# Optimization experiments

Hardware: AMD Instinct MI355X
Metric: run time of the kernel (lower is better)

The kernel has to match this reference:

```python
import jax, jax.numpy as jnp
import numpy as np

NA, NW, H = 20000, 100000, 128
DA, DW = 64, 128
E_CR, E_IN, E_CO = 400000, 600000, 300000


def _seg_softmax(logits, seg, n):
    m = jax.ops.segment_max(logits, seg, num_segments=n)
    e = jnp.exp(logits - m[seg])
    s = jax.ops.segment_sum(e, seg, num_segments=n)
    return e / (s[seg] + 1e-16)


def _gat(x_src, x_dst, edge, W, b, a_s, a_d):
    # PyG GATConv, heads=1, concat=False, shared lin for src/dst, add_self_loops=True
    n_src, n_dst = x_src.shape[0], x_dst.shape[0]
    loops = jnp.arange(min(n_src, n_dst), dtype=edge.dtype)
    src = jnp.concatenate([edge[0], loops])
    dst = jnp.concatenate([edge[1], loops])
    hs = x_src @ W            # [n_src, H]
    hd = x_dst @ W            # [n_dst, H]
    logit = jax.nn.leaky_relu((hs @ a_s)[src] + (hd @ a_d)[dst], 0.2)
    alpha = _seg_softmax(logit, dst, n_dst)          # softmax over in-neighborhoods
    out = jax.ops.segment_sum(alpha[:, None] * hs[src], dst, num_segments=n_dst)
    return out + b


def _mlp2(x, w1, b1, w2, b2):
    return jax.nn.relu(x @ w1 + b1) @ w2 + b2


def setup_inputs() -> dict:
    key = jax.random.key(0)
    ks = iter(jax.random.split(key, 40))

    def p(shape, scale=0.1):
        return jax.random.normal(next(ks), shape, jnp.float32) * scale

    def edges(n_src, n_dst, E):
        s = jax.random.randint(next(ks), (E,), 0, n_src, dtype=jnp.int32)
        d = jax.random.randint(next(ks), (E,), 0, n_dst, dtype=jnp.int32)
        d = jnp.where(s == d, (d + 1) % n_dst, d)  # keep input loop-free (PyG strips them)
        return jnp.stack([s, d])

    e_creates = edges(NA, NW, E_CR)
    inp = {
        'artist_feat': jax.random.normal(next(ks), (NA, DA), jnp.float32),
        'work_feat': jax.random.normal(next(ks), (NW, DW), jnp.float32),
        'a_w1': p((DA, H)), 'a_b1': jnp.zeros(H, jnp.float32),
        'a_w2': p((H, H)), 'a_b2': jnp.zeros(H, jnp.float32),
        'w_w1': p((DW, H)), 'w_b1': jnp.zeros(H, jnp.float32),
        'w_w2': p((H, H)), 'w_b2': jnp.zeros(H, jnp.float32),
        'cr_W': p((H, H)), 'cr_b': jnp.zeros(H, jnp.float32), 'cr_as': p((H,)), 'cr_ad': p((H,)),
        'in_W': p((H, H)), 'in_b': jnp.zeros(H, jnp.float32), 'in_as': p((H,)), 'in_ad': p((H,)),
        'co_W': p((H, H)), 'co_b': jnp.zeros(H, jnp.float32), 'co_as': p((H,)), 'co_ad': p((H,)),
        'p_w1': p((2 * H, 256)), 'p_b1': jnp.zeros(256, jnp.float32),
        'p_w2': p((256, 128)), 'p_b2': jnp.zeros(128, jnp.float32),
        'p_w3': p((128, 1)), 'p_b3': jnp.zeros(1, jnp.float32),
        'e_creates': e_creates,
        'e_created_by': jnp.flip(e_creates, axis=0),  # reverse relation [work, artist]
        'e_infl': edges(NW, NW, E_IN),
        'e_collab': edges(NA, NA, E_CO),
    }
    return inp


def reference(artist_feat, work_feat,
              a_w1, a_b1, a_w2, a_b2,
              w_w1, w_b1, w_w2, w_b2,
              cr_W, cr_b, cr_as, cr_ad,
              in_W, in_b, in_as, in_ad,
              co_W, co_b, co_as, co_ad,
              p_w1, p_b1, p_w2, p_b2, p_w3, p_b3,
              e_creates, e_created_by, e_infl, e_collab):
    ax = _mlp2(artist_feat, a_w1, a_b1, a_w2, a_b2)      # [NA, H]
    wx = _mlp2(work_feat, w_w1, w_b1, w_w2, w_b2)        # [NW, H]
    wx = jax.nn.elu(_gat(ax, wx, e_creates, cr_W, cr_b, cr_as, cr_ad))
    wx = jax.nn.elu(_gat(wx, wx, e_infl, in_W, in_b, in_as, in_ad))
    au = _gat(wx, ax, e_created_by, cr_W, cr_b, cr_as, cr_ad)  # no elu (matches source)
    ac = jax.nn.elu(_gat(au, au, e_collab, co_W, co_b, co_as, co_ad))
    comb = jnp.concatenate([au, ac], axis=1)             # [NA, 2H]
    h = jax.nn.relu(comb @ p_w1 + p_b1)                  # dropout is identity in eval
    h = jax.nn.relu(h @ p_w2 + p_b2)
    return (h @ p_w3 + p_b3).squeeze()
```

## Files before the change

kernel.cpp:

```cpp
#include <hip/hip_runtime.h>
#include <hip/hip_bf16.h>
#include <cstddef>

#define NA 20000
#define NW 100000
#define HH 128
#define DA 64
#define E_CR 400000
#define E_IN 600000
#define E_CO 300000

#define ROW1 0
#define ROW2 (NW)
#define ROW3 (2 * NW)
#define ROW4 (2 * NW + NA)
#define NTOT (2 * NW + 2 * NA)
#define CAPW 40
#define CAPA 88
#define NPREP (10 * 128 + 1)
#define GNB ((NA + 127) / 128)

typedef short v8s __attribute__((ext_vector_type(8)));
typedef float v4f __attribute__((ext_vector_type(4)));

constexpr int PSLOT = 2 * 128 * 264;

__device__ inline short f2bf(float x) {
    union { float f; unsigned u; } c; c.f = x;
    unsigned r = c.u + 0x7fff + ((c.u >> 16) & 1);
    return (short)(r >> 16);
}
__device__ inline float bf2f(short s) {
    union { unsigned u; float f; } c; c.u = ((unsigned)(unsigned short)s) << 16;
    return c.f;
}
__device__ inline float bfu2f(unsigned short s) {
    union { unsigned u; float f; } c; c.u = ((unsigned)s) << 16;
    return c.f;
}

__device__ inline void split8(const float* xv, v8s& h, v8s& l) {
#pragma unroll
    for (int p = 0; p < 4; ++p) {
        float2 xf; xf.x = xv[2 * p]; xf.y = xv[2 * p + 1];
        __hip_bfloat162 hb = __float22bfloat162_rn(xf);
        float2 hf = __bfloat1622float2(hb);
        float2 lf; lf.x = xf.x - hf.x; lf.y = xf.y - hf.y;
        __hip_bfloat162 lb = __float22bfloat162_rn(lf);
        union { __hip_bfloat162 b; short2 s; } uh, ul;
        uh.b = hb; ul.b = lb;
        h[2 * p] = uh.s.x; h[2 * p + 1] = uh.s.y;
        l[2 * p] = ul.s.x; l[2 * p + 1] = ul.s.y;
    }
}

struct AppChunk { const int* e; int E; int* pad; int cap; int* deg; };

__device__ inline void do_append(const AppChunk& ap, int bid) {
    int b0 = bid * 1024 + threadIdx.x;
    int s[4], d[4]; bool ok[4];
#pragma unroll
    for (int u = 0; u < 4; ++u) {
        int i = b0 + u * 256;
        ok[u] = i < ap.E;
        s[u] = 0; d[u] = 0;
        if (ok[u]) { s[u] = ap.e[i]; d[u] = ap.e[ap.E + i]; }
    }
    int p[4];
#pragma unroll
    for (int u = 0; u < 4; ++u) if (ok[u]) p[u] = atomicAdd(&ap.deg[d[u]], 1);
#pragma unroll
    for (int u = 0; u < 4; ++u)
        if (ok[u] && p[u] < ap.cap)
            ap.pad[(size_t)d[u] * ap.cap + p[u]] = s[u];
}

struct PrepDesc { const float* src; int ldw; int K; };
struct PrepArgs {
    PrepDesc d[10]; const float* wvW; const float* wvA; float* vd;
    const float* gX; const float* gB; float* gY; int gM;
};

__global__ __launch_bounds__(256) void k_prep_append(PrepArgs a, short* __restrict__ out,
                                                    AppChunk ap)
{
    __shared__ short Bs2[2 * 128 * 72];
    const int napp = (ap.E + 1023) >> 10;
    int bx = blockIdx.x;
    if (bx < napp) { do_append(ap, bx); return; }
    bx -= napp;
    if (bx < GNB) {
        const int bid = bx;
        const int tid = threadIdx.x;
        const int wave = tid >> 6, lane = tid & 63;
        const int l15 = lane & 15, quad = lane >> 4;
        const int wrow = bid * 128 + wave * 32;
        for (int e = tid; e < 64 * 128; e += 256) {
            int n = e & 127, k = e >> 7;
            float x = a.d[0].src[(size_t)k * 128 + n];
            short h = f2bf(x);
            short l = f2bf(x - bf2f(h));
            Bs2[n * 72 + k] = h;
            Bs2[128 * 72 + n * 72 + k] = l;
        }
        v8s ah[2][2], al[2][2];
#pragma unroll
        for (int rf = 0; rf < 2; ++rf) {
            int r = wrow + rf * 16 + l15; if (r >= a.gM) r = a.gM - 1;
            const float* xp = a.gX + (size_t)r * DA + quad * 8;
#pragma unroll
            for (int kf = 0; kf < 2; ++kf) {
                float xv[8];
                *(float4*)&xv[0] = *(const float4*)(xp + kf * 32);
                *(float4*)&xv[4] = *(const float4*)(xp + kf * 32 + 4);
                split8(xv, ah[rf][kf], al[rf][kf]);
            }
        }
        __syncthreads();
        v4f acc[2][8];
#pragma unroll
        for (int rf = 0; rf < 2; ++rf)
#pragma unroll
            for (int cf = 0; cf < 8; ++cf) acc[rf][cf] = (v4f){0.f, 0.f, 0.f, 0.f};
#pragma unroll
        for (int kf = 0; kf < 2; ++kf) {
#pragma unroll
            for (int cf = 0; cf < 8; ++cf) {
                int coff = (cf * 16 + l15) * 72 + kf * 32 + quad * 8;
                v8s bh = *(const v8s*)&Bs2[coff];
                v8s bl = *(const v8s*)&Bs2[128 * 72 + coff];
#pragma unroll
                for (int rf = 0; rf < 2; ++rf) {
                    acc[rf][cf] = __builtin_amdgcn_mfma_f32_16x16x32_bf16(al[rf][kf], bh, acc[rf][cf], 0, 0, 0);
                    acc[rf][cf] = __builtin_amdgcn_mfma_f32_16x16x32_bf16(ah[rf][kf], bl, acc[rf][cf], 0, 0, 0);
                    acc[rf][cf] = __builtin_amdgcn_mfma_f32_16x16x32_bf16(ah[rf][kf], bh, acc[rf][cf], 0, 0, 0);
                }
            }
        }
        float bv[8];
#pragma unroll
        for (int cf = 0; cf < 8; ++cf) bv[cf] = a.gB[cf * 16 + l15];
#pragma unroll
        for (int rf = 0; rf < 2; ++rf) {
#pragma unroll
            for (int reg = 0; reg < 4; ++reg) {
                int r = wrow + rf * 16 + quad * 4 + reg;
                if (r >= a.gM) continue;
                float* yp = a.gY + (size_t)r * HH;
#pragma unroll
                for (int cf = 0; cf < 8; ++cf) {
                    float o = acc[rf][cf][reg] + bv[cf];
                    yp[cf * 16 + l15] = o > 0.f ? o : 0.f;
                }
            }
        }
        return;
    }
    bx -= GNB;
    if (bx == NPREP - 1) {
        __shared__ float sa[HH];
        int t = threadIdx.x;
        if (t < HH) sa[t] = a.wvA[t];
        __syncthreads();
        if (t < HH) {
            float s = 0.f;
            for (int jj = 0; jj < HH; ++jj) s += a.wvW[(size_t)t * HH + jj] * sa[jj];
            a.vd[t] = s;
        }
        return;
    }
    int m = bx >> 7;
    int e = (bx & 127) * 256 + threadIdx.x;
    PrepDesc dd = a.d[m];
    int K = dd.K;
    int KP = (K <= 128) ? K + 8 : K;
    if (e >= K * 128) return;
    int n = e & 127, k = e >> 7;
    float x = dd.src[(size_t)k * dd.ldw + n];
    short h = f2bf(x);
    short l = f2bf(x - bf2f(h));
    short* base = out + (size_t)m * PSLOT;
    base[n * KP + k] = h;
    base[128 * KP + n * KP + k] = l;
}

template<int K, int ACT, int NSS, int ST, int LDSB, int OBF, int DUAL, int XBF>
__global__ __launch_bounds__(256, 4) void k_mfma(
    const float* __restrict__ X, int ldx,
    const short* __restrict__ Wp,
    const float* __restrict__ bias,
    float* __restrict__ Y, int ldy, int M,
    const float* __restrict__ v1, float* __restrict__ ss1,
    const float* __restrict__ v2, float* __restrict__ ss2,
    const float* __restrict__ sb)
{
    constexpr int KF = K / 32;
    constexpr int KP = (K <= 128) ? K + 8 : K;
    __shared__ short Bs[LDSB ? 2 * 128 * KP : 8];
    const int tid = threadIdx.x;
    const int wave = tid >> 6, lane = tid & 63;
    const int l15 = lane & 15, quad = lane >> 4;
    int bid = blockIdx.x;
    if (DUAL) {
        int g0 = gridDim.x >> 1;
        if (bid >= g0) { bid -= g0; Wp += PSLOT; bias += 128; Y += 128; }
    }
    const int wrow = bid * 128 + wave * 32;

    if (LDSB) {
        const float4* src = (const float4*)Wp;
        float4* dst = (float4*)Bs;
        constexpr int total = 2 * 128 * KP / 8;
        for (int i = tid; i < total; i += 256) dst[i] = src[i];
        __syncthreads();
    }

    v4f acc[2][8];
#pragma unroll
    for (int rf = 0; rf < 2; ++rf)
#pragma unroll
        for (int cf = 0; cf < 8; ++cf) acc[rf][cf] = (v4f){0.f, 0.f, 0.f, 0.f};

    const unsigned short* xb16[2];
    const float* xb32[2];
#pragma unroll
    for (int rf = 0; rf < 2; ++rf) {
        int r = wrow + rf * 16 + l15; if (r >= M) r = M - 1;
        xb16[rf] = (const unsigned short*)X + (size_t)r * ldx + quad * 8;
        xb32[rf] = X + (size_t)r * ldx + quad * 8;
    }

#pragma unroll
    for (int kf = 0; kf < KF; ++kf) {
        v8s ah[2], al[2];
#pragma unroll
        for (int rf = 0; rf < 2; ++rf) {
            if (XBF) {
                ah[rf] = *(const v8s*)(xb16[rf] + kf * 32);
            } else {
                float xv[8];
                *(float4*)&xv[0] = *(const float4*)(xb32[rf] + kf * 32);
                *(float4*)&xv[4] = *(const float4*)(xb32[rf] + kf * 32 + 4);
                split8(xv, ah[rf], al[rf]);
            }
        }
#pragma unroll
        for (int cf = 0; cf < 8; ++cf) {
            const short* bp = LDSB ? &Bs[(cf * 16 + l15) * KP + kf * 32 + quad * 8]
                                   : Wp + (size_t)(cf * 16 + l15) * KP + kf * 32 + quad * 8;
            v8s bh = *(const v8s*)bp;
            v8s bl = *(const v8s*)(bp + 128 * KP);
#pragma unroll
            for (int rf = 0; rf < 2; ++rf) {
                if (!XBF) acc[rf][cf] = __builtin_amdgcn_mfma_f32_16x16x32_bf16(al[rf], bh, acc[rf][cf], 0, 0, 0);
                acc[rf][cf] = __builtin_amdgcn_mfma_f32_16x16x32_bf16(ah[rf], bl, acc[rf][cf], 0, 0, 0);
                acc[rf][cf] = __builtin_amdgcn_mfma_f32_16x16x32_bf16(ah[rf], bh, acc[rf][cf], 0, 0, 0);
            }
        }
    }

    float bv[8], v1c[8], v2c[8];
#pragma unroll
    for (int cf = 0; cf < 8; ++cf) {
        int col = cf * 16 + l15;
        bv[cf] = bias ? bias[col] : 0.f;
        if (NSS >= 1) v1c[cf] = v1[col];
        if (NSS >= 2) v2c[cf] = v2[col];
    }
    float sbv = (NSS >= 1 && sb) ? sb[0] : 0.f;

#pragma unroll
    for (int rf = 0; rf < 2; ++rf) {
#pragma unroll
        for (int reg = 0; reg < 4; ++reg) {
            int r = wrow + rf * 16 + quad * 4 + reg;
            if (r >= M) continue;
            float p1 = 0.f, p2 = 0.f;
#pragma unroll
            for (int cf = 0; cf < 8; ++cf) {
                float o = acc[rf][cf][reg] + bv[cf];
                if (ACT == 1) o = o > 0.f ? o : 0.f;
                if (NSS >= 1) p1 = fmaf(o, v1c[cf], p1);
                if (NSS >= 2) p2 = fmaf(o, v2c[cf], p2);
                if (ST) {
                    if (OBF) ((unsigned short*)Y)[(size_t)r * ldy + cf * 16 + l15] = (unsigned short)f2bf(o);
                    else     Y[(size_t)r * ldy + cf * 16 + l15] = o;
                }
            }
            if (NSS >= 1) {
#pragma unroll
                for (int w = 1; w < 16; w <<= 1) {
                    p1 += __shfl_xor(p1, w, 64);
                    if (NSS >= 2) p2 += __shfl_xor(p2, w, 64);
                }
                if (l15 == 0) {
                    ss1[r] = p1 + sbv;
                    if (NSS >= 2) ss2[r] = p2;
                }
            }
        }
    }
}

struct MfmaCfg {
    const float* X; int ldx;
    const short* Wp;
    const float* bias;
    float* Y; int ldy; int M;
    int act, nss, obf, xbf, st;
    const float* v1; float* ss1;
    const float* v2; float* ss2;
    int nblocks;
};

__global__ __launch_bounds__(256, 4) void k_mfma2(MfmaCfg c0, MfmaCfg c1, AppChunk ap)
{
    constexpr int KF = 4, KP = 136;
    const int napp = (ap.E + 1023) >> 10;
    int bid = blockIdx.x;
    if (bid < napp) { do_append(ap, bid); return; }
    bid -= napp;
    const bool first = bid < c0.nblocks;
    const MfmaCfg& c = first ? c0 : c1;
    if (!first) bid -= c0.nblocks;
    const int tid = threadIdx.x;
    const int wave = tid >> 6, lane = tid & 63;
    const int l15 = lane & 15, quad = lane >> 4;
    const int wrow = bid * 128 + wave * 32;

    v4f acc[2][8];
#pragma unroll
    for (int rf = 0; rf < 2; ++rf)
#pragma unroll
        for (int cf = 0; cf < 8; ++cf) acc[rf][cf] = (v4f){0.f, 0.f, 0.f, 0.f};

    const unsigned short* xb16[2];
    const float* xb32[2];
#pragma unroll
    for (int rf = 0; rf < 2; ++rf) {
        int r = wrow + rf * 16 + l15; if (r >= c.M) r = c.M - 1;
        xb16[rf] = (const unsigned short*)c.X + (size_t)r * c.ldx + quad * 8;
        xb32[rf] = c.X + (size_t)r * c.ldx + quad * 8;
    }

#pragma unroll
    for (int kf = 0; kf < KF; ++kf) {
        v8s ah[2], al[2];
#pragma unroll
        for (int rf = 0; rf < 2; ++rf) {
            if (c.xbf) {
                ah[rf] = *(const v8s*)(xb16[rf] + kf * 32);
                al[rf] = (v8s)(short)0;
            } else {
                float xv[8];
                *(float4*)&xv[0] = *(const float4*)(xb32[rf] + kf * 32);
                *(float4*)&xv[4] = *(const float4*)(xb32[rf] + kf * 32 + 4);
                split8(xv, ah[rf], al[rf]);
            }
        }
#pragma unroll
        for (int cf = 0; cf < 8; ++cf) {
            const short* bp = c.Wp + (size_t)(cf * 16 + l15) * KP + kf * 32 + quad * 8;
            v8s bh = *(const v8s*)bp;
            v8s bl = *(const v8s*)(bp + 128 * KP);
#pragma unroll
            for (int rf = 0; rf < 2; ++rf) {
                if (!c.xbf) acc[rf][cf] = __builtin_amdgcn_mfma_f32_16x16x32_bf16(al[rf], bh, acc[rf][cf], 0, 0, 0);
                acc[rf][cf] = __builtin_amdgcn_mfma_f32_16x16x32_bf16(ah[rf], bl, acc[rf][cf], 0, 0, 0);
                acc[rf][cf] = __builtin_amdgcn_mfma_f32_16x16x32_bf16(ah[rf], bh, acc[rf][cf], 0, 0, 0);
            }
        }
    }

    float bv[8], v1c[8], v2c[8];
#pragma unroll
    for (int cf = 0; cf < 8; ++cf) {
        int col = cf * 16 + l15;
        bv[cf] = c.bias ? c.bias[col] : 0.f;
        v1c[cf] = (c.nss >= 1) ? c.v1[col] : 0.f;
        v2c[cf] = (c.nss >= 2) ? c.v2[col] : 0.f;
    }

#pragma unroll
    for (int rf = 0; rf < 2; ++rf) {
#pragma unroll
        for (int reg = 0; reg < 4; ++reg) {
            int r = wrow + rf * 16 + quad * 4 + reg;
            if (r >= c.M) continue;
            float p1 = 0.f, p2 = 0.f;
#pragma unroll
            for (int cf = 0; cf < 8; ++cf) {
                float o = acc[rf][cf][reg] + bv[cf];
                if (c.act) o = o > 0.f ? o : 0.f;
                p1 = fmaf(o, v1c[cf], p1);
                p2 = fmaf(o, v2c[cf], p2);
                if (c.st) {
                    if (c.obf) ((unsigned short*)c.Y)[(size_t)r * c.ldy + cf * 16 + l15] = (unsigned short)f2bf(o);
                    else       c.Y[(size_t)r * c.ldy + cf * 16 + l15] = o;
                }
            }
            if (c.nss >= 1) {
#pragma unroll
                for (int w = 1; w < 16; w <<= 1) {
                    p1 += __shfl_xor(p1, w, 64);
                    p2 += __shfl_xor(p2, w, 64);
                }
                if (l15 == 0) {
                    c.ss1[r] = p1;
                    if (c.nss >= 2) c.ss2[r] = p2;
                }
            }
        }
    }
}

template<int ELU, int U, int CAP, int OBF>
__global__ __launch_bounds__(256) void k_aggregate(
    const int* __restrict__ deg, const int* __restrict__ esp,
    const unsigned short* __restrict__ hs, const float* __restrict__ ss,
    const float* __restrict__ sd, const float* __restrict__ bias,
    void* __restrict__ out, int ldy, int n, int loopn)
{
    int lane = threadIdx.x & 63;
    int wv = threadIdx.x >> 6;
    int d = blockIdx.x * 4 + wv;
    if (d >= n) return;
    int half = lane >> 5;
    int col = (lane & 31) * 4;
    const int* row = esp + (size_t)d * CAP;
    int i1 = deg[d]; if (i1 > CAP) i1 = CAP;
    float sdv = sd[d];
    float den = 0.f;
    float ax = 0.f, ay = 0.f, az = 0.f, aw = 0.f;
    if (half == 0 && d < loopn) {
        ushort4 h = *(const ushort4*)(hs + (size_t)d * HH + col);
        float l = ss[d] + sdv;
        l = l < 0.f ? 0.2f * l : l;
        float e = __expf(l);
        den += e;
        ax = fmaf(e, bfu2f(h.x), ax);
        ay = fmaf(e, bfu2f(h.y), ay);
        az = fmaf(e, bfu2f(h.z), az);
        aw = fmaf(e, bfu2f(h.w), aw);
    }
    int i = 0;
    for (; i + 2 * U <= i1; i += 2 * U) {
        int s[U]; ushort4 h[U]; float sv[U];
#pragma unroll
        for (int u = 0; u < U; ++u) s[u] = row[i + 2 * u + half];
#pragma unroll
        for (int u = 0; u < U; ++u) h[u] = *(const ushort4*)(hs + (size_t)s[u] * HH + col);
#pragma unroll
        for (int u = 0; u < U; ++u) sv[u] = ss[s[u]];
#pragma unroll
        for (int u = 0; u < U; ++u) {
            float l = sv[u] + sdv;
            l = l < 0.f ? 0.2f * l : l;
            float e = __expf(l);
            den += e;
            ax = fmaf(e, bfu2f(h[u].x), ax);
            ay = fmaf(e, bfu2f(h[u].y), ay);
            az = fmaf(e, bfu2f(h[u].z), az);
            aw = fmaf(e, bfu2f(h[u].w), aw);
        }
    }
    if (i < i1) {
        int s[U]; ushort4 h[U]; float sv[U]; bool act[U];
#pragma unroll
        for (int u = 0; u < U; ++u) {
            int idx = i + 2 * u + half;
            act[u] = idx < i1;
            s[u] = row[act[u] ? idx : (i1 - 1)];
        }
#pragma unroll
        for (int u = 0; u < U; ++u) h[u] = *(const ushort4*)(hs + (size_t)s[u] * HH + col);
#pragma unroll
        for (int u = 0; u < U; ++u) sv[u] = ss[s[u]];
#pragma unroll
        for (int u = 0; u < U; ++u) {
            float l = sv[u] + sdv;
            l = l < 0.f ? 0.2f * l : l;
            float e = act[u] ? __expf(l) : 0.f;
            den += e;
            ax = fmaf(e, bfu2f(h[u].x), ax);
            ay = fmaf(e, bfu2f(h[u].y), ay);
            az = fmaf(e, bfu2f(h[u].z), az);
            aw = fmaf(e, bfu2f(h[u].w), aw);
        }
    }
    den += __shfl_xor(den, 32, 64);
    ax += __shfl_xor(ax, 32, 64);
    ay += __shfl_xor(ay, 32, 64);
    az += __shfl_xor(az, 32, 64);
    aw += __shfl_xor(aw, 32, 64);
    if (half == 0) {
        float4 b = *(const float4*)(bias + col);
        float inv = 1.f / (den + 1e-16f);
        float o0 = ax * inv + b.x;
        float o1 = ay * inv + b.y;
        float o2 = az * inv + b.z;
        float o3 = aw * inv + b.w;
        if (ELU) {
            o0 = o0 > 0.f ? o0 : expm1f(o0);
            o1 = o1 > 0.f ? o1 : expm1f(o1);
            o2 = o2 > 0.f ? o2 : expm1f(o2);
            o3 = o3 > 0.f ? o3 : expm1f(o3);
        }
        if (OBF) {
            ushort4 ob;
            ob.x = (unsigned short)f2bf(o0);
            ob.y = (unsigned short)f2bf(o1);
            ob.z = (unsigned short)f2bf(o2);
            ob.w = (unsigned short)f2bf(o3);
            *(ushort4*)((unsigned short*)out + (size_t)d * ldy + col) = ob;
        } else {
            *(float4*)((float*)out + (size_t)d * ldy + col) = make_float4(o0, o1, o2, o3);
        }
    }
}

extern "C" void kernel_launch(void* const* d_in, const int* in_sizes, int n_in,
                              void* d_out, int out_size, void* d_ws, size_t ws_size,
                              hipStream_t stream)
{
    const float* artist = (const float*)d_in[0];
    const float* workf  = (const float*)d_in[1];
    const float* a_w1 = (const float*)d_in[2];  const float* a_b1 = (const float*)d_in[3];
    const float* a_w2 = (const float*)d_in[4];  const float* a_b2 = (const float*)d_in[5];
    const float* w_w1 = (const float*)d_in[6];  const float* w_b1 = (const float*)d_in[7];
    const float* w_w2 = (const float*)d_in[8];  const float* w_b2 = (const float*)d_in[9];
    const float* cr_W = (const float*)d_in[10]; const float* cr_b = (const float*)d_in[11];
    const float* cr_as = (const float*)d_in[12]; const float* cr_ad = (const float*)d_in[13];
    const float* in_W = (const float*)d_in[14]; const float* in_b = (const float*)d_in[15];
    const float* in_as = (const float*)d_in[16]; const float* in_ad = (const float*)d_in[17];
    const float* co_W = (const float*)d_in[18]; const float* co_b = (const float*)d_in[19];
    const float* co_as = (const float*)d_in[20]; const float* co_ad = (const float*)d_in[21];
    const float* p_w1 = (const float*)d_in[22]; const float* p_b1 = (const float*)d_in[23];
    const float* p_w2 = (const float*)d_in[24]; const float* p_b2 = (const float*)d_in[25];
    const float* p_w3 = (const float*)d_in[26]; const float* p_b3 = (const float*)d_in[27];
    const int* e_cr = (const int*)d_in[28];
    const int* e_cb = (const int*)d_in[29];
    const int* e_in = (const int*)d_in[30];
    const int* e_co = (const int*)d_in[31];

    char* wsp = (char*)d_ws;
    size_t off = 0;
    auto alloc = [&](size_t bytes) -> void* {
        void* p = wsp + off;
        off += (bytes + 255) / 256 * 256;
        return p;
    };
    float* ax   = (float*)alloc((size_t)NA * HH * 4);
    float* hsA  = (float*)alloc((size_t)NA * HH * 4);
    unsigned short* hsw = (unsigned short*)alloc((size_t)NW * HH * 2);
    unsigned short* wxb = (unsigned short*)alloc((size_t)NW * HH * 2);
    unsigned short* hsb = (unsigned short*)alloc((size_t)NW * HH * 2);
    float* h1   = (float*)alloc((size_t)NA * 256 * 4);
    float* comb = (float*)alloc((size_t)NA * 256 * 4);
    float* ss1 = (float*)alloc((size_t)NA * 4);
    float* sd1 = (float*)alloc((size_t)NW * 4);
    float* ss2 = (float*)alloc((size_t)NW * 4);
    float* sd2 = (float*)alloc((size_t)NW * 4);
    float* ss3 = (float*)alloc((size_t)NW * 4);
    float* sd3 = (float*)alloc((size_t)NA * 4);
    float* ss4 = (float*)alloc((size_t)NA * 4);
    float* sd4 = (float*)alloc((size_t)NA * 4);
    float* vd  = (float*)alloc(HH * 4);
    int* deg   = (int*)alloc((size_t)NTOT * 4);
    int* pad1  = (int*)alloc((size_t)NW * CAPW * 4);
    int* pad2  = (int*)alloc((size_t)NW * CAPW * 4);
    int* pad3  = (int*)alloc((size_t)NA * CAPA * 4);
    int* pad4  = (int*)alloc((size_t)NA * CAPA * 4);
    short* preW = (short*)alloc((size_t)10 * PSLOT * 2);
    (void)ws_size; (void)in_sizes; (void)n_in; (void)out_size;

    auto pre = [&](int m) { return preW + (size_t)m * PSLOT; };
    auto gg = [](int M) { return (M + 127) / 128; };
    auto apb = [](int E) { return (E + 1023) / 1024; };
    const float* nf = nullptr;
    float* nfm = nullptr;

    PrepArgs pa;
    pa.d[0] = {a_w1, HH, DA};
    pa.d[1] = {a_w2, HH, HH};
    pa.d[2] = {w_w1, HH, HH};
    pa.d[3] = {w_w2, HH, HH};
    pa.d[4] = {cr_W, HH, HH};
    pa.d[5] = {in_W, HH, HH};
    pa.d[6] = {co_W, HH, HH};
    pa.d[7] = {p_w1, 256, 256};
    pa.d[8] = {p_w1 + 128, 256, 256};
    pa.d[9] = {p_w2, HH, 256};
    pa.wvW = cr_W; pa.wvA = cr_ad; pa.vd = vd;
    pa.gX = artist; pa.gB = a_b1; pa.gY = hsA; pa.gM = NA;

    AppChunk ap1 = {e_cr, E_CR, pad1, CAPW, deg + ROW1};
    AppChunk ap2 = {e_in, E_IN, pad2, CAPW, deg + ROW2};
    AppChunk ap3 = {e_cb, E_CR, pad3, CAPA, deg + ROW3};
    AppChunk ap4 = {e_co, E_CO, pad4, CAPA, deg + ROW4};

    (void)hipMemsetAsync(deg, 0, (size_t)NTOT * 4, stream);

    k_prep_append<<<NPREP + GNB + apb(E_CR), 256, 0, stream>>>(pa, preW, ap1);

    {
        MfmaCfg c0 = {workf, HH, pre(2), w_b1, (float*)hsw, HH, NW, 1, 0, 1, 0, 1, nf, nfm, nf, nfm, gg(NW)};
        MfmaCfg c1 = {hsA, HH, pre(1), a_b2, ax, HH, NA, 0, 1, 0, 0, 1, vd, sd3, nf, nfm, gg(NA)};
        k_mfma2<<<gg(NW) + gg(NA) + apb(E_IN), 256, 0, stream>>>(c0, c1, ap2);
    }
    {
        MfmaCfg c0 = {(const float*)hsw, HH, pre(3), w_b2, nfm, HH, NW, 0, 1, 0, 1, 0, vd, sd1, nf, nfm, gg(NW)};
        MfmaCfg c1 = {ax, HH, pre(4), nullptr, (float*)hsb, HH, NA, 0, 1, 1, 0, 1, cr_as, ss1, nf, nfm, gg(NA)};
        k_mfma2<<<gg(NW) + gg(NA) + apb(E_CR), 256, 0, stream>>>(c0, c1, ap3);
    }

    k_aggregate<1, 2, CAPW, 1><<<(NW + 3) / 4, 256, 0, stream>>>(deg + ROW1, pad1, hsb, ss1, sd1, cr_b, wxb, HH, NW, NA);

    {
        MfmaCfg c0 = {(const float*)wxb, HH, pre(5), nullptr, (float*)hsb, HH, NW, 0, 2, 1, 1, 1, in_as, ss2, in_ad, sd2, gg(NW)};
        MfmaCfg c1 = {nullptr, 0, nullptr, nullptr, nullptr, 0, 0, 0, 0, 0, 0, 0, nf, nfm, nf, nfm, 0};
        k_mfma2<<<gg(NW) + apb(E_CO), 256, 0, stream>>>(c0, c1, ap4);
    }
    k_aggregate<1, 2, CAPW, 1><<<(NW + 3) / 4, 256, 0, stream>>>(deg + ROW2, pad2, hsb, ss2, sd2, in_b, wxb, HH, NW, NW);

    k_mfma<HH, 0, 1, 1, 0, 1, 0, 1><<<gg(NW), 256, 0, stream>>>((const float*)wxb, HH, pre(4), nullptr, (float*)hsb, HH, NW, cr_as, ss3, nf, nfm, nf);
    k_aggregate<0, 4, CAPA, 0><<<(NA + 3) / 4, 256, 0, stream>>>(deg + ROW3, pad3, hsb, ss3, sd3, cr_b, comb, 256, NA, NA);

    k_mfma<HH, 0, 2, 1, 0, 1, 0, 0><<<gg(NA), 256, 0, stream>>>(comb, 256, pre(6), nullptr, (float*)hsb, HH, NA, co_as, ss4, co_ad, sd4, nf);
    k_aggregate<1, 4, CAPA, 0><<<(NA + 3) / 4, 256, 0, stream>>>(deg + ROW4, pad4, hsb, ss4, sd4, co_b, comb + 128, 256, NA, NA);

    k_mfma<256, 1, 0, 1, 0, 0, 1, 0><<<2 * gg(NA), 256, 0, stream>>>(comb, 256, pre(7), p_b1, h1, 256, NA, nf, nfm, nf, nfm, nf);
    k_mfma<256, 1, 1, 0, 0, 0, 0, 0><<<gg(NA), 256, 0, stream>>>(h1, 256, pre(9), p_b2, nfm, 0, NA, p_w3, (float*)d_out, nf, nfm, p_b3);
}
```

Measured before the change: 589.6 us.

## Fold second MLP layers into GAT weights and merge edge appends into prep

Precomputes composed weights (a_w2·cr_W, bias a_b2·cr_W) and attention-dot vectors (w_w2·cr_W·cr_ad, a_w2·vd) so the second MLP layer for artists and works no longer has to be materialised. The work MLP output is reduced directly to a per-row attention score, and the artist path goes straight from the hidden layer to the projected features. All four edge-append passes move into the single prep kernel, which removes a launch and shrinks the later mfma grids. Folding the weights changes the rounding order, and the small serial prep blocks (weight product loops run per thread) could stall the front of the graph.

```diff
diff --git a/kernel.cpp b/kernel.cpp
--- a/kernel.cpp
+++ b/kernel.cpp
@@ -17,8 +17,8 @@
 #define NTOT (2 * NW + 2 * NA)
 #define CAPW 40
 #define CAPA 88
-#define NPREP (10 * 128 + 1)
 #define GNB ((NA + 127) / 128)
+#define NPREPG (7 * 128)
 
 typedef short v8s __attribute__((ext_vector_type(8)));
 typedef float v4f __attribute__((ext_vector_type(4)));
@@ -77,18 +77,86 @@
 
 struct PrepDesc { const float* src; int ldw; int K; };
 struct PrepArgs {
-    PrepDesc d[10]; const float* wvW; const float* wvA; float* vd;
+    PrepDesc d[10];
+    const float *wvW, *wvA;
+    const float *ww2, *aw2, *wb2, *ab2;
+    float *uW, *u3, *cons, *bf;
+    short* wf;
     const float* gX; const float* gB; float* gY; int gM;
 };
 
 __global__ __launch_bounds__(256) void k_prep_append(PrepArgs a, short* __restrict__ out,
-                                                    AppChunk ap)
+        AppChunk ap1, AppChunk ap2, AppChunk ap3, AppChunk ap4)
 {
     __shared__ short Bs2[2 * 128 * 72];
-    const int napp = (ap.E + 1023) >> 10;
     int bx = blockIdx.x;
-    if (bx < napp) { do_append(ap, bx); return; }
-    bx -= napp;
+
+    if (bx == 0) {
+        __shared__ float sv[HH];
+        int t = threadIdx.x;
+        if (t < HH) {
+            float s = 0.f;
+            for (int j = 0; j < HH; ++j) s += a.wvW[(size_t)t * HH + j] * a.wvA[j];
+            sv[t] = s;
+        }
+        __syncthreads();
+        if (t < HH) {
+            float s = 0.f;
+            for (int j = 0; j < HH; ++j) s += a.ww2[(size_t)t * HH + j] * sv[j];
+            a.uW[t] = s;
+        } else {
+            int k = t - HH;
+            float s = 0.f;
+            for (int j = 0; j < HH; ++j) s += a.aw2[(size_t)k * HH + j] * sv[j];
+            a.u3[k] = s;
+        }
+        if (t == 0) {
+            float s = 0.f;
+            for (int j = 0; j < HH; ++j) s += a.wb2[j] * sv[j];
+            a.cons[0] = s;
+        }
+        if (t == 1) {
+            float s = 0.f;
+            for (int j = 0; j < HH; ++j) s += a.ab2[j] * sv[j];
+            a.cons[1] = s;
+        }
+        return;
+    }
+    bx -= 1;
+    if (bx < 4) {
+        int k = bx * 32 + (threadIdx.x >> 3);
+        int cb = (threadIdx.x & 7) * 16;
+        for (int c = cb; c < cb + 16; ++c) {
+            float s = 0.f;
+            for (int j = 0; j < HH; ++j) s += a.aw2[(size_t)k * HH + j] * a.wvW[(size_t)j * HH + c];
+            short h = f2bf(s);
+            short l = f2bf(s - bf2f(h));
+            a.wf[c * 136 + k] = h;
+            a.wf[128 * 136 + c * 136 + k] = l;
+        }
+        if (bx == 0 && threadIdx.x < HH) {
+            int c = threadIdx.x;
+            float s = 0.f;
+            for (int j = 0; j < HH; ++j) s += a.ab2[j] * a.wvW[(size_t)j * HH + c];
+            a.bf[c] = s;
+        }
+        return;
+    }
+    bx -= 4;
+    {
+        int n1 = (ap1.E + 1023) >> 10;
+        if (bx < n1) { do_append(ap1, bx); return; }
+        bx -= n1;
+        int n2 = (ap2.E + 1023) >> 10;
+        if (bx < n2) { do_append(ap2, bx); return; }
+        bx -= n2;
+        int n3 = (ap3.E + 1023) >> 10;
+        if (bx < n3) { do_append(ap3, bx); return; }
+        bx -= n3;
+        int n4 = (ap4.E + 1023) >> 10;
+        if (bx < n4) { do_append(ap4, bx); return; }
+        bx -= n4;
+    }
     if (bx < GNB) {
         const int bid = bx;
         const int tid = threadIdx.x;
@@ -157,19 +225,8 @@
         return;
     }
     bx -= GNB;
-    if (bx == NPREP - 1) {
-        __shared__ float sa[HH];
-        int t = threadIdx.x;
-        if (t < HH) sa[t] = a.wvA[t];
-        __syncthreads();
-        if (t < HH) {
-            float s = 0.f;
-            for (int jj = 0; jj < HH; ++jj) s += a.wvW[(size_t)t * HH + jj] * sa[jj];
-            a.vd[t] = s;
-        }
-        return;
-    }
-    int m = bx >> 7;
+    constexpr int smap[7] = {2, 4, 5, 6, 7, 8, 9};
+    int m = smap[bx >> 7];
     int e = (bx & 127) * 256 + threadIdx.x;
     PrepDesc dd = a.d[m];
     int K = dd.K;
@@ -310,16 +367,15 @@
     int act, nss, obf, xbf, st;
     const float* v1; float* ss1;
     const float* v2; float* ss2;
+    const float* sb1;
+    const float* vx; float* ssx; const float* cx;
     int nblocks;
 };
 
-__global__ __launch_bounds__(256, 4) void k_mfma2(MfmaCfg c0, MfmaCfg c1, AppChunk ap)
+__global__ __launch_bounds__(256, 4) void k_mfma2(MfmaCfg c0, MfmaCfg c1)
 {
     constexpr int KF = 4, KP = 136;
-    const int napp = (ap.E + 1023) >> 10;
     int bid = blockIdx.x;
-    if (bid < napp) { do_append(ap, bid); return; }
-    bid -= napp;
     const bool first = bid < c0.nblocks;
     const MfmaCfg& c = first ? c0 : c1;
     if (!first) bid -= c0.nblocks;
@@ -343,9 +399,15 @@
         xb32[rf] = c.X + (size_t)r * c.ldx + quad * 8;
     }
 
+    float px[2] = {0.f, 0.f};
 #pragma unroll
     for (int kf = 0; kf < KF; ++kf) {
         v8s ah[2], al[2];
+        float uv[8];
+        if (c.vx) {
+            *(float4*)&uv[0] = *(const float4*)(c.vx + kf * 32 + quad * 8);
+            *(float4*)&uv[4] = *(const float4*)(c.vx + kf * 32 + quad * 8 + 4);
+        }
 #pragma unroll
         for (int rf = 0; rf < 2; ++rf) {
             if (c.xbf) {
@@ -356,6 +418,10 @@
                 *(float4*)&xv[0] = *(const float4*)(xb32[rf] + kf * 32);
                 *(float4*)&xv[4] = *(const float4*)(xb32[rf] + kf * 32 + 4);
                 split8(xv, ah[rf], al[rf]);
+                if (c.vx) {
+#pragma unroll
+                    for (int j = 0; j < 8; ++j) px[rf] = fmaf(xv[j], uv[j], px[rf]);
+                }
             }
         }
 #pragma unroll
@@ -369,6 +435,18 @@
                 acc[rf][cf] = __builtin_amdgcn_mfma_f32_16x16x32_bf16(ah[rf], bl, acc[rf][cf], 0, 0, 0);
                 acc[rf][cf] = __builtin_amdgcn_mfma_f32_16x16x32_bf16(ah[rf], bh, acc[rf][cf], 0, 0, 0);
             }
+        }
+    }
+
+    if (c.vx) {
+        float cxv = c.cx ? c.cx[0] : 0.f;
+#pragma unroll
+        for (int rf = 0; rf < 2; ++rf) {
+            float p = px[rf];
+            p += __shfl_xor(p, 16, 64);
+            p += __shfl_xor(p, 32, 64);
+            int rr = wrow + rf * 16 + l15;
+            if (quad == 0 && rr < c.M) c.ssx[rr] = p + cxv;
         }
     }
 
@@ -380,6 +458,7 @@
         v1c[cf] = (c.nss >= 1) ? c.v1[col] : 0.f;
         v2c[cf] = (c.nss >= 2) ? c.v2[col] : 0.f;
     }
+    float sbv = (c.nss >= 1 && c.sb1) ? c.sb1[0] : 0.f;
 
 #pragma unroll
     for (int rf = 0; rf < 2; ++rf) {
@@ -406,7 +485,7 @@
                     p2 += __shfl_xor(p2, w, 64);
                 }
                 if (l15 == 0) {
-                    c.ss1[r] = p1;
+                    c.ss1[r] = p1 + sbv;
                     if (c.nss >= 2) c.ss2[r] = p2;
                 }
             }
@@ -550,9 +629,7 @@
         off += (bytes + 255) / 256 * 256;
         return p;
     };
-    float* ax   = (float*)alloc((size_t)NA * HH * 4);
     float* hsA  = (float*)alloc((size_t)NA * HH * 4);
-    unsigned short* hsw = (unsigned short*)alloc((size_t)NW * HH * 2);
     unsigned short* wxb = (unsigned short*)alloc((size_t)NW * HH * 2);
     unsigned short* hsb = (unsigned short*)alloc((size_t)NW * HH * 2);
     float* h1   = (float*)alloc((size_t)NA * 256 * 4);
@@ -565,7 +642,10 @@
     float* sd3 = (float*)alloc((size_t)NA * 4);
     float* ss4 = (float*)alloc((size_t)NA * 4);
     float* sd4 = (float*)alloc((size_t)NA * 4);
-    float* vd  = (float*)alloc(HH * 4);
+    float* uW  = (float*)alloc(HH * 4);
+    float* u3v = (float*)alloc(HH * 4);
+    float* bfv = (float*)alloc(HH * 4);
+    float* cons = (float*)alloc(2 * 4);
     int* deg   = (int*)alloc((size_t)NTOT * 4);
     int* pad1  = (int*)alloc((size_t)NW * CAPW * 4);
     int* pad2  = (int*)alloc((size_t)NW * CAPW * 4);
@@ -591,7 +671,10 @@
     pa.d[7] = {p_w1, 256, 256};
     pa.d[8] = {p_w1 + 128, 256, 256};
     pa.d[9] = {p_w2, HH, 256};
-    pa.wvW = cr_W; pa.wvA = cr_ad; pa.vd = vd;
+    pa.wvW = cr_W; pa.wvA = cr_ad;
+    pa.ww2 = w_w2; pa.aw2 = a_w2; pa.wb2 = w_b2; pa.ab2 = a_b2;
+    pa.uW = uW; pa.u3 = u3v; pa.cons = cons; pa.bf = bfv;
+    pa.wf = pre(1);
     pa.gX = artist; pa.gB = a_b1; pa.gY = hsA; pa.gM = NA;
 
     AppChunk ap1 = {e_cr, E_CR, pad1, CAPW, deg + ROW1};
@@ -601,26 +684,30 @@
 
     (void)hipMemsetAsync(deg, 0, (size_t)NTOT * 4, stream);
 
-    k_prep_append<<<NPREP + GNB + apb(E_CR), 256, 0, stream>>>(pa, preW, ap1);
-
     {
-        MfmaCfg c0 = {workf, HH, pre(2), w_b1, (float*)hsw, HH, NW, 1, 0, 1, 0, 1, nf, nfm, nf, nfm, gg(NW)};
-        MfmaCfg c1 = {hsA, HH, pre(1), a_b2, ax, HH, NA, 0, 1, 0, 0, 1, vd, sd3, nf, nfm, gg(NA)};
-        k_mfma2<<<gg(NW) + gg(NA) + apb(E_IN), 256, 0, stream>>>(c0, c1, ap2);
-    }
+        int nblk = 5 + apb(E_CR) + apb(E_IN) + apb(E_CR) + apb(E_CO) + GNB + NPREPG;
+        k_prep_append<<<nblk, 256, 0, stream>>>(pa, preW, ap1, ap2, ap3, ap4);
+    }
+
     {
-        MfmaCfg c0 = {(const float*)hsw, HH, pre(3), w_b2, nfm, HH, NW, 0, 1, 0, 1, 0, vd, sd1, nf, nfm, gg(NW)};
-        MfmaCfg c1 = {ax, HH, pre(4), nullptr, (float*)hsb, HH, NA, 0, 1, 1, 0, 1, cr_as, ss1, nf, nfm, gg(NA)};
-        k_mfma2<<<gg(NW) + gg(NA) + apb(E_CR), 256, 0, stream>>>(c0, c1, ap3);
+        MfmaCfg c0 = {workf, HH, pre(2), w_b1, nullptr, HH, NW,
+                      1, 1, 0, 0, 0,
+                      uW, sd1, nf, nfm,
+                      cons,
+                      nf, nfm, nf,
+                      gg(NW)};
+        MfmaCfg c1 = {hsA, HH, pre(1), bfv, (float*)hsb, HH, NA,
+                      0, 1, 1, 0, 1,
+                      cr_as, ss1, nf, nfm,
+                      nf,
+                      u3v, sd3, cons + 1,
+                      gg(NA)};
+        k_mfma2<<<gg(NW) + gg(NA), 256, 0, stream>>>(c0, c1);
     }
 
     k_aggregate<1, 2, CAPW, 1><<<(NW + 3) / 4, 256, 0, stream>>>(deg + ROW1, pad1, hsb, ss1, sd1, cr_b, wxb, HH, NW, NA);
 
-    {
-        MfmaCfg c0 = {(const float*)wxb, HH, pre(5), nullptr, (float*)hsb, HH, NW, 0, 2, 1, 1, 1, in_as, ss2, in_ad, sd2, gg(NW)};
-        MfmaCfg c1 = {nullptr, 0, nullptr, nullptr, nullptr, 0, 0, 0, 0, 0, 0, 0, nf, nfm, nf, nfm, 0};
-        k_mfma2<<<gg(NW) + apb(E_CO), 256, 0, stream>>>(c0, c1, ap4);
-    }
+    k_mfma<HH, 0, 2, 1, 0, 1, 0, 1><<<gg(NW), 256, 0, stream>>>((const float*)wxb, HH, pre(5), nullptr, (float*)hsb, HH, NW, in_as, ss2, in_ad, sd2, nf);
     k_aggregate<1, 2, CAPW, 1><<<(NW + 3) / 4, 256, 0, stream>>>(deg + ROW2, pad2, hsb, ss2, sd2, in_b, wxb, HH, NW, NW);
 
     k_mfma<HH, 0, 1, 1, 0, 1, 0, 1><<<gg(NW), 256, 0, stream>>>((const float*)wxb, HH, pre(4), nullptr, (float*)hsb, HH, NW, cr_as, ss3, nf, nfm, nf);
```

After: 705.0 us. 19.6% more time.
